# Optimization experiments

Hardware: AMD Instinct MI355X
Metric: run time of the kernel (lower is better)

Reference implementation:

```python
import jax, jax.numpy as jnp
import numpy as np

N_HEADS = 16  # must match init_kwargs
BIAS_SCALE = 0.1


def _src_grid(out_size, in_size):
    # torch F.interpolate bilinear, align_corners=False semantics
    scale = in_size / out_size
    src = jnp.clip((jnp.arange(out_size, dtype=jnp.float32) + 0.5) * scale - 0.5, 0.0)
    i0 = jnp.minimum(jnp.floor(src).astype(jnp.int32), in_size - 1)
    i1 = jnp.minimum(i0 + 1, in_size - 1)
    w = src - i0.astype(jnp.float32)
    return i0, i1, w


def _bilinear_resize(img, out_h, out_w):
    Hin, Win = img.shape[-2], img.shape[-1]
    r0, r1, wy = _src_grid(out_h, Hin)
    c0, c1, wx = _src_grid(out_w, Win)
    rows = img[:, r0, :] * (1.0 - wy)[None, :, None] + img[:, r1, :] * wy[None, :, None]
    return rows[:, :, c0] * (1.0 - wx)[None, None, :] + rows[:, :, c1] * wx[None, None, :]


def setup_inputs() -> dict:
    key = jax.random.key(0)
    ks = jax.random.split(key, 10)
    B, L, D, M, K = 4, 1024, 1024, 64, 32
    s = 0.02
    return {
        "x": jax.random.normal(ks[0], (B, L, D), dtype=jnp.float32),
        "harmonics": jax.random.normal(ks[1], (B, M, K), dtype=jnp.float32),
        "wq": jax.random.normal(ks[2], (D, D), dtype=jnp.float32) * s,
        "bq": jax.random.normal(ks[3], (D,), dtype=jnp.float32) * s,
        "wk": jax.random.normal(ks[4], (D, D), dtype=jnp.float32) * s,
        "bk": jax.random.normal(ks[5], (D,), dtype=jnp.float32) * s,
        "wv": jax.random.normal(ks[6], (D, D), dtype=jnp.float32) * s,
        "bv": jax.random.normal(ks[7], (D,), dtype=jnp.float32) * s,
        "wo": jax.random.normal(ks[8], (D, D), dtype=jnp.float32) * s,
        "bo": jax.random.normal(ks[9], (D,), dtype=jnp.float32) * s,
    }


def reference(x, harmonics, wq, bq, wk, bk, wv, bv, wo, bo):
    B, L, D = x.shape
    hd = D // N_HEADS
    scaling = hd ** -0.5

    def split_heads(t):  # [B, L, D] -> [B, H, L, hd]
        return t.reshape(B, L, N_HEADS, hd).transpose(0, 2, 1, 3)

    q = split_heads(x @ wq.T + bq)
    k = split_heads(x @ wk.T + bk)
    v = split_heads(x @ wv.T + bv)

    scores = jnp.einsum("bhqd,bhkd->bhqk", q, k) * scaling  # [B, H, L, L]

    gram = jnp.einsum("bmk,bnk->bmn", harmonics, harmonics)  # [B, M, M]
    bias = _bilinear_resize(gram, L, L)  # [B, L, L]
    scores = scores + BIAS_SCALE * bias[:, None, :, :]

    attn = jax.nn.softmax(scores, axis=-1)
    out = jnp.einsum("bhqk,bhkd->bhqd", attn, v)  # [B, H, L, hd]
    out = out.transpose(0, 2, 1, 3).reshape(B, L, D)
    return out @ wo.T + bo
```

## Files before the change

### kernel.cpp

```cpp
#include <hip/hip_runtime.h>


using short8  = __attribute__((ext_vector_type(8))) short;
using short4v = __attribute__((ext_vector_type(4))) short;
using float4v = __attribute__((ext_vector_type(4))) float;

#define MFMA16(a, b, c) __builtin_amdgcn_mfma_f32_16x16x32_bf16((a), (b), (c), 0, 0, 0)

#define LOG2E 1.44269504088896f

static __device__ __forceinline__ short f2bf(float f) {
    union { float f; unsigned u; } v; v.f = f;
    unsigned r = v.u + 0x7fffu + ((v.u >> 16) & 1u);
    return (short)(r >> 16);
}

static __device__ __forceinline__ unsigned pack2bf(float lo, float hi) {
    union { float f; unsigned u; } a, b;
    a.f = lo; b.f = hi;
    return __builtin_amdgcn_perm(b.u + 0x8000u, a.u + 0x8000u, 0x07060302u);
}

static __device__ __forceinline__ void dma16(const short* g, short* l) {
    __builtin_amdgcn_global_load_lds((const __attribute__((address_space(1))) void*)g,
                                     (__attribute__((address_space(3))) void*)l, 16, 0, 0);
}

__global__ __launch_bounds__(256) void convert_all(
    const float* __restrict__ x,  const float* __restrict__ wq,
    const float* __restrict__ wk, const float* __restrict__ wv,
    const float* __restrict__ wo, short* __restrict__ xb, short* __restrict__ wb) {
    int idx = blockIdx.x * 256 + threadIdx.x;
    for (int i = idx; i < 2097152; i += gridDim.x * 256) {
        const float* src; short* dst;
        if (i < 1048576) {
            src = x + (size_t)i * 4;
            dst = xb + (size_t)i * 4;
        } else {
            int j = i - 1048576;
            int sel = j >> 18;
            const float* w = (sel == 0) ? wq : (sel == 1) ? wk : (sel == 2) ? wv : wo;
            src = w + (size_t)(j & 262143) * 4;
            dst = wb + (size_t)j * 4;
        }
        float4v v = *(const float4v*)src;
        short4v o;
        o.x = f2bf(v.x); o.y = f2bf(v.y); o.z = f2bf(v.z); o.w = f2bf(v.w);
        *(short4v*)dst = o;
    }
}

__global__ __launch_bounds__(256) void fill_aug(const float* __restrict__ harm,
                                                short* __restrict__ Qp,
                                                short* __restrict__ Kp) {
    int b  = blockIdx.y;
    int lc = blockIdx.x;
    int tid = threadIdx.x;
    int ll = tid >> 3;
    int d8 = (tid & 7) * 8;
    int l  = lc * 32 + ll;

    __shared__ float hs[64][33];
    for (int i = tid; i < 2048; i += 256) hs[i >> 5][i & 31] = harm[(size_t)b * 2048 + i];
    __syncthreads();

    float src = (l + 0.5f) * 0.0625f - 0.5f;
    if (src < 0.f) src = 0.f;
    int r0 = (int)floorf(src); if (r0 > 63) r0 = 63;
    int r1 = r0 + 1;           if (r1 > 63) r1 = 63;
    float wy = src - (float)r0;

    float hr[32];
    #pragma unroll
    for (int k = 0; k < 32; k++) hr[k] = (1.f - wy) * hs[r0][k] + wy * hs[r1][k];

    short8 qa, ka;
    #pragma unroll
    for (int j = 0; j < 8; j++) {
        float g = 0.f;
        #pragma unroll
        for (int k = 0; k < 32; k++) g += hr[k] * hs[d8 + j][k];
        qa[j] = f2bf(0.1f * LOG2E * g);
    }
    #pragma unroll
    for (int j = 0; j < 8; j++) {
        float vv = 0.f;
        if (d8 + j == r0) vv += 1.f - wy;
        if (d8 + j == r1) vv += wy;
        ka[j] = f2bf(vv);
    }
    for (int h = 0; h < 16; h++) {
        size_t base = (((size_t)(b * 16 + h) * 1024 + l) << 7) + 64 + d8;
        *(short8*)(Qp + base) = qa;
        *(short8*)(Kp + base) = ka;
    }
}

template <int MODE>
__global__ __launch_bounds__(256, 2) void gemm_kernel(
    const short* __restrict__ A,
    const short* __restrict__ Wb,
    const float* __restrict__ B0, const float* __restrict__ B1, const float* __restrict__ B2,
    short* __restrict__ Qp, short* __restrict__ Kp, short* __restrict__ Vp,
    float* __restrict__ outF) {
    const int z = blockIdx.z;
    const short* W  = Wb + (size_t)z * 1048576;
    const float* Bs = (z == 0) ? B0 : ((z == 1) ? B1 : B2);

    __shared__ short Sm[2][8192];

    const int tid  = threadIdx.x;
    const int lane = tid & 63;
    const int wv   = tid >> 6;
    const int wm   = (wv >> 1) * 64;
    const int wn   = (wv & 1) * 64;
    const int l16  = lane & 15;
    const int quad = lane >> 4;
    const int bm   = blockIdx.x * 128;
    const int bn   = blockIdx.y * 128;

    const short* aSrc[2];
    const short* wSrc[2];
    #pragma unroll
    for (int j = 0; j < 2; j++) {
        int c = j * 256 + tid;
        int r = c >> 2, gs = (c & 3) ^ ((r >> 1) & 3);
        aSrc[j] = A + (size_t)(bm + r) * 1024 + gs * 8;
        wSrc[j] = W + (size_t)(bn + r) * 1024 + gs * 8;
    }
    const int fr = (quad ^ ((l16 >> 1) & 3)) * 8;
    int ai[4], bi[4];
    #pragma unroll
    for (int t = 0; t < 4; t++) {
        ai[t] = (wm + t * 16 + l16) * 32 + fr;
        bi[t] = 4096 + (wn + t * 16 + l16) * 32 + fr;
    }

    float4v zero4 = {0.f, 0.f, 0.f, 0.f};
    float4v acc[4][4];
    #pragma unroll
    for (int i = 0; i < 4; i++)
        #pragma unroll
        for (int j = 0; j < 4; j++) acc[i][j] = zero4;

    dma16(aSrc[0], &Sm[0][wv * 512]);
    dma16(aSrc[1], &Sm[0][2048 + wv * 512]);
    dma16(wSrc[0], &Sm[0][4096 + wv * 512]);
    dma16(wSrc[1], &Sm[0][6144 + wv * 512]);
    #pragma unroll
    for (int j = 0; j < 2; j++) { aSrc[j] += 32; wSrc[j] += 32; }
    __syncthreads();

    for (int kt = 0; kt < 32; kt++) {
        const int cur = kt & 1, nxt = cur ^ 1;
        if (kt < 31) {
            dma16(aSrc[0], &Sm[nxt][wv * 512]);
            dma16(aSrc[1], &Sm[nxt][2048 + wv * 512]);
            dma16(wSrc[0], &Sm[nxt][4096 + wv * 512]);
            dma16(wSrc[1], &Sm[nxt][6144 + wv * 512]);
            #pragma unroll
            for (int j = 0; j < 2; j++) { aSrc[j] += 32; wSrc[j] += 32; }
        }

        short8 af[4], bfr[4];
        #pragma unroll
        for (int mt = 0; mt < 4; mt++) af[mt]  = *(const short8*)&Sm[cur][ai[mt]];
        #pragma unroll
        for (int nt = 0; nt < 4; nt++) bfr[nt] = *(const short8*)&Sm[cur][bi[nt]];
        #pragma unroll
        for (int mt = 0; mt < 4; mt++)
            #pragma unroll
            for (int nt = 0; nt < 4; nt++)
                acc[mt][nt] = MFMA16(af[mt], bfr[nt], acc[mt][nt]);

        __syncthreads();
    }

    #pragma unroll
    for (int mt = 0; mt < 4; mt++)
        #pragma unroll
        for (int nt = 0; nt < 4; nt++) {
            int col = bn + wn + nt * 16 + l16;
            float bias = Bs[col];
            #pragma unroll
            for (int r = 0; r < 4; r++) {
                int row = bm + wm + mt * 16 + quad * 4 + r;
                float val = acc[mt][nt][r] + bias;
                if (MODE == 1) {
                    outF[(size_t)row * 1024 + col] = val;
                } else {
                    int b = row >> 10, l = row & 1023;
                    int h = col >> 6,  d = col & 63;
                    size_t bhl = (size_t)(b * 16 + h) * 1024 + l;
                    if (z == 0)      Qp[(bhl << 7) + d] = f2bf(val * (0.125f * LOG2E));
                    else if (z == 1) Kp[(bhl << 7) + d] = f2bf(val);
                    else {
                        int slot = (l & ~31) | (((l >> 2) & 3) << 3) |
                                   (((l >> 4) & 1) << 2) | (l & 3);
                        Vp[(((size_t)(b * 16 + h) * 64 + d) << 10) + slot] = f2bf(val);
                    }
                }
            }
        }
}

__global__ __attribute__((amdgpu_flat_work_group_size(512, 512),
                          amdgpu_waves_per_eu(4, 4)))
void flash_kernel(const short* __restrict__ Qp,
                  const short* __restrict__ Kp,
                  const short* __restrict__ Vp,
                  short* __restrict__ AO) {
    const int h  = blockIdx.x;
    const int qb = blockIdx.y;
    const int b  = blockIdx.z;
    const int tid  = threadIdx.x;
    const int lane = tid & 63;
    const int w    = tid >> 6;
    const int l16  = lane & 15;
    const int quad = lane >> 4;
    const size_t bh = (size_t)(b * 16 + h);

    __shared__ short Ks[16384];
    __shared__ short Vs[8192];

    short8 qf[4];
    {
        const short* Qb = Qp + ((bh * 1024 + qb * 128 + w * 16 + l16) << 7) + quad * 8;
        #pragma unroll
        for (int c = 0; c < 4; c++) qf[c] = *(const short8*)(Qb + c * 32);
    }

    const short* kSrc[2];
    #pragma unroll
    for (int jj = 0; jj < 2; jj++) {
        int key = (w * 2 + jj) * 4 + quad;
        kSrc[jj] = Kp + (bh << 17) + key * 128 + ((l16 ^ (key & 15)) * 8);
    }
    const short* vSrc;
    {
        int d = w * 8 + (lane >> 3);
        vSrc = Vp + (bh << 16) + d * 1024 + (((lane & 7) ^ (d & 7)) * 8);
    }

    int krd[4];
    #pragma unroll
    for (int c = 0; c < 4; c++) krd[c] = l16 * 128 + (((c * 4 + quad) ^ l16) * 8);
    int vrd[2];
    #pragma unroll
    for (int g = 0; g < 2; g++) vrd[g] = l16 * 64 + (((g * 4 + quad) ^ (l16 & 7)) * 8);

    #pragma unroll
    for (int jj = 0; jj < 2; jj++) dma16(kSrc[jj], &Ks[w * 1024 + jj * 512]);
    dma16(vSrc, &Vs[w * 512]);
    #pragma unroll
    for (int jj = 0; jj < 2; jj++) kSrc[jj] += 8192;
    vSrc += 64;
    int dstK = 8192, dstV = 4096;

    float4v zero4 = {0.f, 0.f, 0.f, 0.f};
    float4v o_acc[4];
    #pragma unroll
    for (int mt = 0; mt < 4; mt++) o_acc[mt] = zero4;
    float l_part = 0.f;

    __syncthreads();

    for (int kt = 0; kt < 16; kt++) {
        if (kt < 15) {
            #pragma unroll
            for (int jj = 0; jj < 2; jj++) dma16(kSrc[jj], &Ks[dstK + w * 1024 + jj * 512]);
            dma16(vSrc, &Vs[dstV + w * 512]);
            #pragma unroll
            for (int jj = 0; jj < 2; jj++) kSrc[jj] += 8192;
            vSrc += 64;
            dstK ^= 8192; dstV ^= 4096;
        }

        float4v s[4];
        #pragma unroll
        for (int mt = 0; mt < 4; mt++) {
            short8 kf[4];
            #pragma unroll
            for (int c = 0; c < 4; c++) kf[c] = *(const short8*)&Ks[krd[c] + mt * 2048];
            s[mt] = zero4;
            #pragma unroll
            for (int c = 0; c < 4; c++)
                s[mt] = MFMA16(kf[c], qf[c], s[mt]);
        }

        #pragma unroll
        for (int mt = 0; mt < 4; mt++)
            #pragma unroll
            for (int r = 0; r < 4; r++) {
                float p = __builtin_exp2f(s[mt][r]);
                s[mt][r] = p;
                l_part += p;
            }

        #pragma unroll
        for (int g = 0; g < 2; g++) {
            short8 pf;
            #pragma unroll
            for (int j = 0; j < 4; j++) {
                ((unsigned*)&pf)[j >> 1] = 0;
            }
            union { unsigned u[4]; short8 v; } t;
            t.u[0] = pack2bf(s[2 * g][0], s[2 * g][1]);
            t.u[1] = pack2bf(s[2 * g][2], s[2 * g][3]);
            t.u[2] = pack2bf(s[2 * g + 1][0], s[2 * g + 1][1]);
            t.u[3] = pack2bf(s[2 * g + 1][2], s[2 * g + 1][3]);
            pf = t.v;
            #pragma unroll
            for (int mt = 0; mt < 4; mt++) {
                short8 vf = *(const short8*)&Vs[vrd[g] + mt * 1024];
                o_acc[mt] = MFMA16(vf, pf, o_acc[mt]);
            }
        }

        if (kt < 15) __syncthreads();
        #pragma unroll
        for (int c = 0; c < 4; c++) krd[c] ^= 8192;
        #pragma unroll
        for (int g = 0; g < 2; g++) vrd[g] ^= 4096;
    }

    {
        float l = l_part;
        l += __shfl_xor(l, 16, 64);
        l += __shfl_xor(l, 32, 64);
        float inv = 1.0f / l;
        int row = b * 1024 + qb * 128 + w * 16 + l16;
        #pragma unroll
        for (int mt = 0; mt < 4; mt++) {
            short4v ov;
            #pragma unroll
            for (int r = 0; r < 4; r++) ov[r] = f2bf(o_acc[mt][r] * inv);
            *(short4v*)(AO + (size_t)row * 1024 + h * 64 + mt * 16 + quad * 4) = ov;
        }
    }
}

extern "C" void kernel_launch(void* const* d_in, const int* in_sizes, int n_in,
                              void* d_out, int out_size, void* d_ws, size_t ws_size,
                              hipStream_t stream) {
    const float* x    = (const float*)d_in[0];
    const float* harm = (const float*)d_in[1];
    const float* wq   = (const float*)d_in[2];
    const float* bq   = (const float*)d_in[3];
    const float* wk   = (const float*)d_in[4];
    const float* bk   = (const float*)d_in[5];
    const float* wv   = (const float*)d_in[6];
    const float* bv   = (const float*)d_in[7];
    const float* wo   = (const float*)d_in[8];
    const float* bo   = (const float*)d_in[9];
    float* outF = (float*)d_out;

    short* xb   = (short*)d_ws;
    short* Qp   = xb + (size_t)4 * 1048576;
    short* Kp   = Qp + (size_t)8 * 1048576;
    short* Vp   = Kp + (size_t)8 * 1048576;
    short* Wqkv = Vp + (size_t)4 * 1048576;
    short* Wob  = Wqkv + (size_t)3 * 1048576;
    short* AO   = xb;

    convert_all<<<dim3(2048), dim3(256), 0, stream>>>(x, wq, wk, wv, wo, xb, Wqkv);
    gemm_kernel<0><<<dim3(32, 8, 3), dim3(256), 0, stream>>>(
        xb, Wqkv, bq, bk, bv, Qp, Kp, Vp, nullptr);
    fill_aug<<<dim3(32, 4), dim3(256), 0, stream>>>(harm, Qp, Kp);
    flash_kernel<<<dim3(16, 8, 4), dim3(512), 0, stream>>>(Qp, Kp, Vp, AO);
    gemm_kernel<1><<<dim3(32, 8, 1), dim3(256), 0, stream>>>(
        AO, Wob, bo, nullptr, nullptr, nullptr, nullptr, nullptr, outF);
}
```

Before: 192.2 us.

## Process two query sub-tiles per wave in flash kernel with 256-thread blocks

The flash attention kernel now runs 4 waves per block instead of 8, and each wave handles 32 query rows (two 16-row sub-tiles). Every K and V fragment read from LDS feeds two MFMAs, which halves LDS read traffic per unit of compute. Each wave now issues twice as many DMA loads per tile. The cost is roughly doubled accumulator and score register use and fewer waves per block, with launch bounds changed to 256 threads and 2 blocks per CU, which may lower occupancy and latency hiding.

```diff
diff --git a/kernel.cpp b/kernel.cpp
--- a/kernel.cpp
+++ b/kernel.cpp
@@ -204,8 +204,7 @@
         }
 }
 
-__global__ __attribute__((amdgpu_flat_work_group_size(512, 512),
-                          amdgpu_waves_per_eu(4, 4)))
+__global__ __launch_bounds__(256, 2)
 void flash_kernel(const short* __restrict__ Qp,
                   const short* __restrict__ Kp,
                   const short* __restrict__ Vp,
@@ -223,23 +222,25 @@
     __shared__ short Ks[16384];
     __shared__ short Vs[8192];
 
-    short8 qf[4];
-    {
-        const short* Qb = Qp + ((bh * 1024 + qb * 128 + w * 16 + l16) << 7) + quad * 8;
-        #pragma unroll
-        for (int c = 0; c < 4; c++) qf[c] = *(const short8*)(Qb + c * 32);
-    }
-
-    const short* kSrc[2];
-    #pragma unroll
-    for (int jj = 0; jj < 2; jj++) {
-        int key = (w * 2 + jj) * 4 + quad;
+    short8 qf[2][4];
+    #pragma unroll
+    for (int u = 0; u < 2; u++) {
+        const short* Qb = Qp + ((bh * 1024 + qb * 128 + w * 32 + u * 16 + l16) << 7) + quad * 8;
+        #pragma unroll
+        for (int c = 0; c < 4; c++) qf[u][c] = *(const short8*)(Qb + c * 32);
+    }
+
+    const short* kSrc[4];
+    #pragma unroll
+    for (int jj = 0; jj < 4; jj++) {
+        int key = w * 16 + jj * 4 + quad;
         kSrc[jj] = Kp + (bh << 17) + key * 128 + ((l16 ^ (key & 15)) * 8);
     }
-    const short* vSrc;
-    {
-        int d = w * 8 + (lane >> 3);
-        vSrc = Vp + (bh << 16) + d * 1024 + (((lane & 7) ^ (d & 7)) * 8);
+    const short* vSrc[2];
+    #pragma unroll
+    for (int g = 0; g < 2; g++) {
+        int d = w * 16 + g * 8 + (lane >> 3);
+        vSrc[g] = Vp + (bh << 16) + d * 1024 + (((lane & 7) ^ (d & 7)) * 8);
     }
 
     int krd[4];
@@ -250,70 +251,82 @@
     for (int g = 0; g < 2; g++) vrd[g] = l16 * 64 + (((g * 4 + quad) ^ (l16 & 7)) * 8);
 
     #pragma unroll
-    for (int jj = 0; jj < 2; jj++) dma16(kSrc[jj], &Ks[w * 1024 + jj * 512]);
-    dma16(vSrc, &Vs[w * 512]);
-    #pragma unroll
-    for (int jj = 0; jj < 2; jj++) kSrc[jj] += 8192;
-    vSrc += 64;
+    for (int jj = 0; jj < 4; jj++) dma16(kSrc[jj], &Ks[w * 2048 + jj * 512]);
+    #pragma unroll
+    for (int g = 0; g < 2; g++) dma16(vSrc[g], &Vs[w * 1024 + g * 512]);
+    #pragma unroll
+    for (int jj = 0; jj < 4; jj++) kSrc[jj] += 8192;
+    #pragma unroll
+    for (int g = 0; g < 2; g++) vSrc[g] += 64;
     int dstK = 8192, dstV = 4096;
 
     float4v zero4 = {0.f, 0.f, 0.f, 0.f};
-    float4v o_acc[4];
-    #pragma unroll
-    for (int mt = 0; mt < 4; mt++) o_acc[mt] = zero4;
-    float l_part = 0.f;
+    float4v o_acc[2][4];
+    #pragma unroll
+    for (int u = 0; u < 2; u++)
+        #pragma unroll
+        for (int mt = 0; mt < 4; mt++) o_acc[u][mt] = zero4;
+    float l_part[2] = {0.f, 0.f};
 
     __syncthreads();
 
     for (int kt = 0; kt < 16; kt++) {
         if (kt < 15) {
             #pragma unroll
-            for (int jj = 0; jj < 2; jj++) dma16(kSrc[jj], &Ks[dstK + w * 1024 + jj * 512]);
-            dma16(vSrc, &Vs[dstV + w * 512]);
-            #pragma unroll
-            for (int jj = 0; jj < 2; jj++) kSrc[jj] += 8192;
-            vSrc += 64;
+            for (int jj = 0; jj < 4; jj++) dma16(kSrc[jj], &Ks[dstK + w * 2048 + jj * 512]);
+            #pragma unroll
+            for (int g = 0; g < 2; g++) dma16(vSrc[g], &Vs[dstV + w * 1024 + g * 512]);
+            #pragma unroll
+            for (int jj = 0; jj < 4; jj++) kSrc[jj] += 8192;
+            #pragma unroll
+            for (int g = 0; g < 2; g++) vSrc[g] += 64;
             dstK ^= 8192; dstV ^= 4096;
         }
 
-        float4v s[4];
+        float4v s[2][4];
         #pragma unroll
         for (int mt = 0; mt < 4; mt++) {
             short8 kf[4];
             #pragma unroll
             for (int c = 0; c < 4; c++) kf[c] = *(const short8*)&Ks[krd[c] + mt * 2048];
-            s[mt] = zero4;
-            #pragma unroll
-            for (int c = 0; c < 4; c++)
-                s[mt] = MFMA16(kf[c], qf[c], s[mt]);
-        }
-
-        #pragma unroll
-        for (int mt = 0; mt < 4; mt++)
-            #pragma unroll
-            for (int r = 0; r < 4; r++) {
-                float p = __builtin_exp2f(s[mt][r]);
-                s[mt][r] = p;
-                l_part += p;
+            #pragma unroll
+            for (int u = 0; u < 2; u++) {
+                s[u][mt] = MFMA16(kf[0], qf[u][0], zero4);
+                #pragma unroll
+                for (int c = 1; c < 4; c++)
+                    s[u][mt] = MFMA16(kf[c], qf[u][c], s[u][mt]);
             }
+        }
+
+        #pragma unroll
+        for (int u = 0; u < 2; u++)
+            #pragma unroll
+            for (int mt = 0; mt < 4; mt++)
+                #pragma unroll
+                for (int r = 0; r < 4; r++) {
+                    float p = __builtin_exp2f(s[u][mt][r]);
+                    s[u][mt][r] = p;
+                    l_part[u] += p;
+                }
 
         #pragma unroll
         for (int g = 0; g < 2; g++) {
-            short8 pf;
-            #pragma unroll
-            for (int j = 0; j < 4; j++) {
-                ((unsigned*)&pf)[j >> 1] = 0;
+            short8 pf[2];
+            #pragma unroll
+            for (int u = 0; u < 2; u++) {
+                union { unsigned uu[4]; short8 v; } t;
+                t.uu[0] = pack2bf(s[u][2 * g][0], s[u][2 * g][1]);
+                t.uu[1] = pack2bf(s[u][2 * g][2], s[u][2 * g][3]);
+                t.uu[2] = pack2bf(s[u][2 * g + 1][0], s[u][2 * g + 1][1]);
+                t.uu[3] = pack2bf(s[u][2 * g + 1][2], s[u][2 * g + 1][3]);
+                pf[u] = t.v;
             }
-            union { unsigned u[4]; short8 v; } t;
-            t.u[0] = pack2bf(s[2 * g][0], s[2 * g][1]);
-            t.u[1] = pack2bf(s[2 * g][2], s[2 * g][3]);
-            t.u[2] = pack2bf(s[2 * g + 1][0], s[2 * g + 1][1]);
-            t.u[3] = pack2bf(s[2 * g + 1][2], s[2 * g + 1][3]);
-            pf = t.v;
             #pragma unroll
             for (int mt = 0; mt < 4; mt++) {
                 short8 vf = *(const short8*)&Vs[vrd[g] + mt * 1024];
-                o_acc[mt] = MFMA16(vf, pf, o_acc[mt]);
+                #pragma unroll
+                for (int u = 0; u < 2; u++)
+                    o_acc[u][mt] = MFMA16(vf, pf[u], o_acc[u][mt]);
             }
         }
 
@@ -324,17 +337,18 @@
         for (int g = 0; g < 2; g++) vrd[g] ^= 4096;
     }
 
-    {
-        float l = l_part;
+    #pragma unroll
+    for (int u = 0; u < 2; u++) {
+        float l = l_part[u];
         l += __shfl_xor(l, 16, 64);
         l += __shfl_xor(l, 32, 64);
         float inv = 1.0f / l;
-        int row = b * 1024 + qb * 128 + w * 16 + l16;
+        int row = b * 1024 + qb * 128 + w * 32 + u * 16 + l16;
         #pragma unroll
         for (int mt = 0; mt < 4; mt++) {
             short4v ov;
             #pragma unroll
-            for (int r = 0; r < 4; r++) ov[r] = f2bf(o_acc[mt][r] * inv);
+            for (int r = 0; r < 4; r++) ov[r] = f2bf(o_acc[u][mt][r] * inv);
             *(short4v*)(AO + (size_t)row * 1024 + h * 64 + mt * 16 + quad * 4) = ov;
         }
     }
@@ -367,7 +381,7 @@
     gemm_kernel<0><<<dim3(32, 8, 3), dim3(256), 0, stream>>>(
         xb, Wqkv, bq, bk, bv, Qp, Kp, Vp, nullptr);
     fill_aug<<<dim3(32, 4), dim3(256), 0, stream>>>(harm, Qp, Kp);
-    flash_kernel<<<dim3(16, 8, 4), dim3(512), 0, stream>>>(Qp, Kp, Vp, AO);
+    flash_kernel<<<dim3(16, 8, 4), dim3(256), 0, stream>>>(Qp, Kp, Vp, AO);
     gemm_kernel<1><<<dim3(32, 8, 1), dim3(256), 0, stream>>>(
         AO, Wob, bo, nullptr, nullptr, nullptr, nullptr, nullptr, outF);
 }
```

New measurement: 192.9 us. No clear change (+0.4%).
